# Performance work log

Measured on AMD Instinct MI355X. Metric: run time of the kernel, lower is better.

## Reference

```python
import jax, jax.numpy as jnp
import numpy as np

NDIM = 3
RADIUS = 0.14
MAX_GRID_DIM = 96
MAX_COLLISIONS = 128
B, N, M, C = 4, 4096, 4096, 16


def setup_inputs() -> dict:
    key = jax.random.key(0)
    k1, k2, k3 = jax.random.split(key, 3)
    locs = jax.random.uniform(k1, (B, N, NDIM), dtype=jnp.float32)
    data = jax.random.normal(k2, (B, N, C), dtype=jnp.float32)
    qlocs = jax.random.uniform(k3, (B, M, NDIM), dtype=jnp.float32)
    return {"locs": locs, "data": data, "qlocs": qlocs}


def _hashgrid_idxs(locs, radius, max_grid_dim):
    """Replicates hashgrid_order: assign each particle a flat grid-cell ID and
    return the permutation (new -> old index) that sorts particles by cell."""
    lower = locs.min(axis=1)                                   # [B,D]
    upper = locs.max(axis=1)                                   # [B,D]
    grid_dims = jnp.ceil(jnp.clip((upper - lower) / radius, 0.0, max_grid_dim))
    center = (lower + upper) * 0.5
    lower = center - grid_dims * radius * 0.5                  # grid lower corner
    cell = jnp.floor((locs - lower[:, None, :]) / radius)
    cell = jnp.clip(cell, 0.0, grid_dims[:, None, :] - 1.0).astype(jnp.int32)
    gd = jnp.maximum(grid_dims.astype(jnp.int32), 1)           # [B,D]
    # row-major strides per batch: stride[d] = prod(gd[d+1:])
    rev = jnp.cumprod(gd[:, ::-1], axis=1)[:, ::-1]            # [B,D]
    strides = jnp.concatenate(
        [rev[:, 1:], jnp.ones((gd.shape[0], 1), jnp.int32)], axis=1)
    cell_ids = (cell * strides[:, None, :]).sum(-1)            # [B,N]
    # stable sort by cell id -> idxs[b, i] = original index of particle now at i
    idxs = jnp.argsort(cell_ids, axis=1)
    return idxs


def reference(locs, data, qlocs):
    idxs = _hashgrid_idxs(locs, RADIUS, MAX_GRID_DIM)
    locs_r = jnp.take_along_axis(locs, idxs[..., None], axis=1)   # [B,N,D]
    data_r = jnp.take_along_axis(data, idxs[..., None], axis=1)   # [B,N,C]

    # Radius search of qlocs against the cell-sorted particles. Neighbor indices
    # are w.r.t. the reordered locs, listed in ascending reordered-index order
    # (cell order), capped at MAX_COLLISIONS, padded with -1.
    qn = (qlocs * qlocs).sum(-1)                                  # [B,M]
    pn = (locs_r * locs_r).sum(-1)                                # [B,N]
    cross = jnp.einsum('bmd,bnd->bmn', qlocs, locs_r)             # [B,M,N]
    dist2 = qn[:, :, None] + pn[:, None, :] - 2.0 * cross         # [B,M,N]
    mask = dist2 <= RADIUS * RADIUS
    # stable argsort of ~mask puts in-radius particles first, in index order
    order = jnp.argsort(~mask, axis=-1)
    neighbors = order[..., :MAX_COLLISIONS].astype(jnp.int32)     # [B,M,K]
    count = mask.sum(-1)                                          # [B,M]
    valid = jnp.arange(MAX_COLLISIONS) < count[..., None]
    neighbors = jnp.where(valid, neighbors, jnp.int32(-1))
    return locs_r, data_r, idxs.astype(jnp.int32), neighbors
```

## Files before the change

### kernel.cpp

```cpp
#include <hip/hip_runtime.h>
#include <stdint.h>

#define BB 4
#define NN 4096
#define MM 4096
#define CC 16
#define KMAX 128

static constexpr int LOCSR_OFF = 0;
static constexpr int DATAR_OFF = BB * NN * 3;
static constexpr int IDXS_OFF  = DATAR_OFF + BB * NN * CC;
static constexpr int NB_OFF    = IDXS_OFF + BB * NN;

static constexpr float RAD_F = 0.14f;
static constexpr float R2F   = (float)(0.14 * 0.14);

__global__ void __launch_bounds__(1024) k_bbox(const float* __restrict__ locs,
                                               float* __restrict__ gp) {
    int b = blockIdx.x;
    __shared__ float smn[3][1024], smx[3][1024];
    int t = threadIdx.x;
    float mn[3] = {1e30f, 1e30f, 1e30f}, mx[3] = {-1e30f, -1e30f, -1e30f};
    const float* base = locs + b * NN * 3;
    for (int i = t; i < NN; i += 1024) {
        for (int d = 0; d < 3; ++d) {
            float v = base[i * 3 + d];
            mn[d] = fminf(mn[d], v);
            mx[d] = fmaxf(mx[d], v);
        }
    }
    for (int d = 0; d < 3; ++d) { smn[d][t] = mn[d]; smx[d][t] = mx[d]; }
    __syncthreads();
    for (int s = 512; s > 0; s >>= 1) {
        if (t < s) {
            for (int d = 0; d < 3; ++d) {
                smn[d][t] = fminf(smn[d][t], smn[d][t + s]);
                smx[d][t] = fmaxf(smx[d][t], smx[d][t + s]);
            }
        }
        __syncthreads();
    }
    if (t == 0) {
        float low2[3], gdf[3];
        int gdi[3];
        for (int d = 0; d < 3; ++d) {
            float lo = smn[d][0], up = smx[d][0];
            float u = __fdiv_rn(__fsub_rn(up, lo), RAD_F);
            u = fminf(fmaxf(u, 0.0f), 96.0f);
            float g = ceilf(u);
            float center = __fmul_rn(__fadd_rn(lo, up), 0.5f);
            low2[d] = __fsub_rn(center, __fmul_rn(__fmul_rn(g, RAD_F), 0.5f));
            gdf[d] = g;
            gdi[d] = max((int)g, 1);
        }
        float* o = gp + b * 8;
        o[0] = low2[0]; o[1] = low2[1]; o[2] = low2[2];
        o[3] = gdf[0];  o[4] = gdf[1];  o[5] = gdf[2];
        ((int*)o)[6] = gdi[1] * gdi[2];
        ((int*)o)[7] = gdi[2];
    }
}

__global__ void k_cellid(const float* __restrict__ locs, const float* __restrict__ gp,
                         int* __restrict__ cid) {
    int idx = blockIdx.x * 256 + threadIdx.x;
    int b = idx >> 12;
    int i = idx & (NN - 1);
    const float* o = gp + b * 8;
    int s0 = ((const int*)o)[6], s1 = ((const int*)o)[7];
    int cc[3];
    for (int d = 0; d < 3; ++d) {
        float x = locs[(b * NN + i) * 3 + d];
        float c = floorf(__fdiv_rn(__fsub_rn(x, o[d]), RAD_F));
        c = fminf(fmaxf(c, 0.0f), __fsub_rn(o[3 + d], 1.0f));
        cc[d] = (int)c;
    }
    cid[b * NN + i] = cc[0] * s0 + cc[1] * s1 + cc[2];
}

__global__ void __launch_bounds__(1024) k_rank(const float* __restrict__ locs,
                                               const float* __restrict__ data,
                                               const int* __restrict__ cid,
                                               float* __restrict__ out,
                                               float4* __restrict__ sp4) {
    __shared__ int4 keys4[NN / 4];
    __shared__ int partial[16][64];
    __shared__ int s_dst[64];
    int blk = blockIdx.x;
    int b = blk >> 6;
    int t = threadIdx.x;
    int wave = t >> 6, lane = t & 63;
    const int4* kg = (const int4*)(cid + b * NN);
    keys4[t] = kg[t];
    __syncthreads();
    int i = (blk & 63) * 64 + lane;
    int key = ((const int*)keys4)[i];
    int rank = 0;
    int j0 = wave * 64;
#pragma unroll 4
    for (int j4 = j0; j4 < j0 + 64; ++j4) {
        int4 kv = keys4[j4];
        int jb = j4 * 4;
        rank += (kv.x < key) || (kv.x == key && (jb    ) < i);
        rank += (kv.y < key) || (kv.y == key && (jb + 1) < i);
        rank += (kv.z < key) || (kv.z == key && (jb + 2) < i);
        rank += (kv.w < key) || (kv.w == key && (jb + 3) < i);
    }
    partial[wave][lane] = rank;
    __syncthreads();
    if (wave == 0) {
        int r = 0;
#pragma unroll
        for (int w = 0; w < 16; ++w) r += partial[w][lane];
        s_dst[lane] = r;
    }
    __syncthreads();
    if (wave == 0) {
        int src = b * NN + i;
        int dst = b * NN + s_dst[lane];
        float x = locs[src * 3 + 0], y = locs[src * 3 + 1], z = locs[src * 3 + 2];
        out[IDXS_OFF + dst] = (float)i;
        out[LOCSR_OFF + dst * 3 + 0] = x;
        out[LOCSR_OFF + dst * 3 + 1] = y;
        out[LOCSR_OFF + dst * 3 + 2] = z;
        float pn = __fadd_rn(__fadd_rn(__fmul_rn(x, x), __fmul_rn(y, y)), __fmul_rn(z, z));
        sp4[dst] = make_float4(x, y, z, pn);
    } else if (wave <= 4) {
        int p = lane;
        int ii = (blk & 63) * 64 + p;
        int dst = b * NN + s_dst[p];
        int c = wave - 1;
        const float4* dsrc = (const float4*)(data + (b * NN + ii) * 16);
        float4* ddst = (float4*)(out + DATAR_OFF + dst * 16);
        ddst[c] = dsrc[c];
    }
}

__global__ void __launch_bounds__(1024) k_neighbors(const float* __restrict__ qlocs,
                                                    const float4* __restrict__ sp4,
                                                    float* __restrict__ out) {
    __shared__ float4 sp[NN];
    int b = blockIdx.x >> 8;
    int t = threadIdx.x;
    const float4* src = sp4 + b * NN;
    for (int k = t; k < NN; k += 1024) sp[k] = src[k];
    __syncthreads();
    int wave = t >> 6, lane = t & 63;
    int m = (blockIdx.x & 255) * 16 + wave;
    const float* q = qlocs + (b * MM + m) * 3;
    float q0 = q[0], q1 = q[1], q2 = q[2];
    float qn = __fadd_rn(__fadd_rn(__fmul_rn(q0, q0), __fmul_rn(q1, q1)), __fmul_rn(q2, q2));
    float* nb = out + NB_OFF + (b * MM + m) * KMAX;
    int count = 0;
    for (int c = 0; c < NN / 64; ++c) {
        int p = c * 64 + lane;
        float4 P = sp[p];
        float cross = fmaf(q2, P.z, fmaf(q1, P.y, __fmul_rn(q0, P.x)));
        float dist2 = __fsub_rn(__fadd_rn(qn, P.w), __fmul_rn(2.0f, cross));
        bool hit = dist2 <= R2F;
        unsigned long long bal = __ballot(hit);
        if (hit) {
            int pos = count + __popcll(bal & ((1ull << lane) - 1ull));
            if (pos < KMAX) nb[pos] = (float)p;
        }
        count += __popcll(bal);
        if (count >= KMAX) break;
    }
    for (int j = count + lane; j < KMAX; j += 64) nb[j] = -1.0f;
}

extern "C" void kernel_launch(void* const* d_in, const int* in_sizes, int n_in,
                              void* d_out, int out_size, void* d_ws, size_t ws_size,
                              hipStream_t stream) {
    const float* locs  = (const float*)d_in[0];
    const float* data  = (const float*)d_in[1];
    const float* qlocs = (const float*)d_in[2];
    float* out = (float*)d_out;
    char* ws = (char*)d_ws;
    float*  gp  = (float*)ws;
    int*    cid = (int*)(ws + 256);
    float4* sp4 = (float4*)(ws + 256 + BB * NN * sizeof(int));

    k_bbox<<<BB, 1024, 0, stream>>>(locs, gp);
    k_cellid<<<(BB * NN) / 256, 256, 0, stream>>>(locs, gp, cid);
    k_rank<<<BB * 64, 1024, 0, stream>>>(locs, data, cid, out, sp4);
    k_neighbors<<<BB * 256, 1024, 0, stream>>>(qlocs, sp4, out);
}
```

Before: 106.2 us.

## Replace brute-force neighbor scan with hash-grid cell-range search

Instead of testing each query against all 4096 sorted particles, a new kernel builds a cell-start table by binary search over the sorted cell ids. The neighbor kernel then visits only the 3x3 columns of cells around each query, scanning contiguous z-ranges in ascending cell order. This keeps the required index-ordered output while doing far less distance work per query. It also moves to smaller blocks reading particles from global memory instead of shared memory, and adds one small kernel launch plus workspace for the cell table.

```diff
diff --git a/kernel.cpp b/kernel.cpp
--- a/kernel.cpp
+++ b/kernel.cpp
@@ -14,6 +14,9 @@
 
 static constexpr float RAD_F = 0.14f;
 static constexpr float R2F   = (float)(0.14 * 0.14);
+
+static constexpr int MAXC    = 96 * 96 * 96;
+static constexpr int CSTRIDE = MAXC + 8;
 
 __global__ void __launch_bounds__(1024) k_bbox(const float* __restrict__ locs,
                                                float* __restrict__ gp) {
@@ -53,11 +56,15 @@
             gdf[d] = g;
             gdi[d] = max((int)g, 1);
         }
-        float* o = gp + b * 8;
+        float* o = gp + b * 12;
         o[0] = low2[0]; o[1] = low2[1]; o[2] = low2[2];
         o[3] = gdf[0];  o[4] = gdf[1];  o[5] = gdf[2];
-        ((int*)o)[6] = gdi[1] * gdi[2];
-        ((int*)o)[7] = gdi[2];
+        ((int*)o)[6]  = gdi[1] * gdi[2];
+        ((int*)o)[7]  = gdi[2];
+        ((int*)o)[8]  = gdi[0] * gdi[1] * gdi[2];
+        ((int*)o)[9]  = gdi[0];
+        ((int*)o)[10] = gdi[1];
+        ((int*)o)[11] = gdi[2];
     }
 }
 
@@ -66,7 +73,7 @@
     int idx = blockIdx.x * 256 + threadIdx.x;
     int b = idx >> 12;
     int i = idx & (NN - 1);
-    const float* o = gp + b * 8;
+    const float* o = gp + b * 12;
     int s0 = ((const int*)o)[6], s1 = ((const int*)o)[7];
     int cc[3];
     for (int d = 0; d < 3; ++d) {
@@ -82,7 +89,8 @@
                                                const float* __restrict__ data,
                                                const int* __restrict__ cid,
                                                float* __restrict__ out,
-                                               float4* __restrict__ sp4) {
+                                               float4* __restrict__ sp4,
+                                               int* __restrict__ cs_sorted) {
     __shared__ int4 keys4[NN / 4];
     __shared__ int partial[16][64];
     __shared__ int s_dst[64];
@@ -123,6 +131,7 @@
         out[LOCSR_OFF + dst * 3 + 0] = x;
         out[LOCSR_OFF + dst * 3 + 1] = y;
         out[LOCSR_OFF + dst * 3 + 2] = z;
+        cs_sorted[dst] = key;
         float pn = __fadd_rn(__fadd_rn(__fmul_rn(x, x), __fmul_rn(y, y)), __fmul_rn(z, z));
         sp4[dst] = make_float4(x, y, z, pn);
     } else if (wave <= 4) {
@@ -136,36 +145,78 @@
     }
 }
 
-__global__ void __launch_bounds__(1024) k_neighbors(const float* __restrict__ qlocs,
-                                                    const float4* __restrict__ sp4,
-                                                    float* __restrict__ out) {
-    __shared__ float4 sp[NN];
-    int b = blockIdx.x >> 8;
-    int t = threadIdx.x;
-    const float4* src = sp4 + b * NN;
-    for (int k = t; k < NN; k += 1024) sp[k] = src[k];
-    __syncthreads();
-    int wave = t >> 6, lane = t & 63;
-    int m = (blockIdx.x & 255) * 16 + wave;
+__global__ void __launch_bounds__(256) k_cellstart(const int* __restrict__ cs_sorted,
+                                                   const float* __restrict__ gp,
+                                                   int* __restrict__ cell_start) {
+    int b = blockIdx.y;
+    int nc = ((const int*)(gp + b * 12))[8];
+    const int* cs = cs_sorted + b * NN;
+    int* cst = cell_start + b * CSTRIDE;
+    for (int c = blockIdx.x * 256 + threadIdx.x; c <= nc; c += gridDim.x * 256) {
+        int lo = 0, hi = NN;
+        while (lo < hi) {
+            int mid = (lo + hi) >> 1;
+            if (cs[mid] < c) lo = mid + 1; else hi = mid;
+        }
+        cst[c] = lo;
+    }
+}
+
+__device__ inline void axis_range(float qd, float lo, int gd, int* c0, int* c1) {
+    const float DL = RAD_F + 1e-4f;
+    float vlo = (qd - DL - lo) / RAD_F;
+    float vhi = (qd + DL - lo) / RAD_F;
+    int a = (int)floorf(vlo), b = (int)floorf(vhi);
+    *c0 = min(max(a, 0), gd - 1);
+    *c1 = min(max(b, 0), gd - 1);
+}
+
+__global__ void __launch_bounds__(256, 8) k_neighbors(const float* __restrict__ qlocs,
+                                                      const float4* __restrict__ sp4,
+                                                      const int* __restrict__ cell_start,
+                                                      const float* __restrict__ gp,
+                                                      float* __restrict__ out) {
+    int blk = blockIdx.x;
+    int b = blk >> 10;
+    int wave = threadIdx.x >> 6, lane = threadIdx.x & 63;
+    int m = (blk & 1023) * 4 + wave;
+    const float* o = gp + b * 12;
+    const int* oi = (const int*)o;
+    int s0 = oi[6], s1 = oi[7];
+    int gd0 = oi[9], gd1 = oi[10], gd2 = oi[11];
     const float* q = qlocs + (b * MM + m) * 3;
     float q0 = q[0], q1 = q[1], q2 = q[2];
     float qn = __fadd_rn(__fadd_rn(__fmul_rn(q0, q0), __fmul_rn(q1, q1)), __fmul_rn(q2, q2));
+    int cx0, cx1, cy0, cy1, cz0, cz1;
+    axis_range(q0, o[0], gd0, &cx0, &cx1);
+    axis_range(q1, o[1], gd1, &cy0, &cy1);
+    axis_range(q2, o[2], gd2, &cz0, &cz1);
+    const float4* sp = sp4 + b * NN;
+    const int* cst = cell_start + b * CSTRIDE;
     float* nb = out + NB_OFF + (b * MM + m) * KMAX;
     int count = 0;
-    for (int c = 0; c < NN / 64; ++c) {
-        int p = c * 64 + lane;
-        float4 P = sp[p];
-        float cross = fmaf(q2, P.z, fmaf(q1, P.y, __fmul_rn(q0, P.x)));
-        float dist2 = __fsub_rn(__fadd_rn(qn, P.w), __fmul_rn(2.0f, cross));
-        bool hit = dist2 <= R2F;
-        unsigned long long bal = __ballot(hit);
-        if (hit) {
-            int pos = count + __popcll(bal & ((1ull << lane) - 1ull));
-            if (pos < KMAX) nb[pos] = (float)p;
-        }
-        count += __popcll(bal);
-        if (count >= KMAX) break;
-    }
+    for (int cx = cx0; cx <= cx1; ++cx) {
+        for (int cy = cy0; cy <= cy1; ++cy) {
+            int base = cx * s0 + cy * s1;
+            int ps = cst[base + cz0];
+            int pe = cst[base + cz1 + 1];
+            for (int p0 = ps; p0 < pe; p0 += 64) {
+                int p = p0 + lane;
+                float4 P = sp[p];
+                float cross = fmaf(q2, P.z, fmaf(q1, P.y, __fmul_rn(q0, P.x)));
+                float dist2 = __fsub_rn(__fadd_rn(qn, P.w), __fmul_rn(2.0f, cross));
+                bool hit = (p < pe) && (dist2 <= R2F);
+                unsigned long long bal = __ballot(hit);
+                if (hit) {
+                    int pos = count + __popcll(bal & ((1ull << lane) - 1ull));
+                    if (pos < KMAX) nb[pos] = (float)p;
+                }
+                count += __popcll(bal);
+                if (count >= KMAX) goto done;
+            }
+        }
+    }
+done:
     for (int j = count + lane; j < KMAX; j += 64) nb[j] = -1.0f;
 }
 
@@ -177,12 +228,15 @@
     const float* qlocs = (const float*)d_in[2];
     float* out = (float*)d_out;
     char* ws = (char*)d_ws;
-    float*  gp  = (float*)ws;
-    int*    cid = (int*)(ws + 256);
-    float4* sp4 = (float4*)(ws + 256 + BB * NN * sizeof(int));
+    float* gp        = (float*)ws;
+    int*   cid       = (int*)(ws + 512);
+    int*   cs_sorted = (int*)(ws + 512 + 65536);
+    float4* sp4      = (float4*)(ws + 512 + 2 * 65536);
+    int*   cell_start = (int*)(ws + 512 + 2 * 65536 + BB * NN * sizeof(float4));
 
     k_bbox<<<BB, 1024, 0, stream>>>(locs, gp);
     k_cellid<<<(BB * NN) / 256, 256, 0, stream>>>(locs, gp, cid);
-    k_rank<<<BB * 64, 1024, 0, stream>>>(locs, data, cid, out, sp4);
-    k_neighbors<<<BB * 256, 1024, 0, stream>>>(qlocs, sp4, out);
-}
+    k_rank<<<BB * 64, 1024, 0, stream>>>(locs, data, cid, out, sp4, cs_sorted);
+    k_cellstart<<<dim3(32, BB), 256, 0, stream>>>(cs_sorted, gp, cell_start);
+    k_neighbors<<<BB * 1024, 256, 0, stream>>>(qlocs, sp4, cell_start, gp, out);
+}
```

New measurement: 100.1 us. 5.8% less time.
